# Kernel optimization log

Hardware: AMD Instinct MI355X
Metric: run time of the kernel (lower is better)

## Reference

```python
import jax, jax.numpy as jnp
import numpy as np

EPS = 1e-6

def rmsnorm(x, w):
    # x * rsqrt(mean(x^2, -1) + eps) * w
    ms = jnp.mean(jnp.square(x), axis=-1, keepdims=True)
    return w * (x * jax.lax.rsqrt(ms + EPS))

def setup_inputs() -> dict:
    key = jax.random.key(0)
    ks = jax.random.split(key, 10)
    B, L, T, D, R = 4, 8, 2048, 1024, 64
    h_base = jax.random.normal(ks[0], (B, T, D), dtype=jnp.float32)
    prev_states = jax.random.normal(ks[1], (B, L, T, D), dtype=jnp.float32)
    query = jax.random.normal(ks[2], (D,), dtype=jnp.float32) * 0.02
    gate = jnp.float32(0.5)
    score_w = jnp.ones((D,), dtype=jnp.float32)
    out_w = jnp.ones((D,), dtype=jnp.float32)
    qnorm_w = jnp.ones((D,), dtype=jnp.float32)
    # low-rank query projections (nn.Linear weight layout: [out, in])
    Wd = jax.random.normal(ks[3], (R, D), dtype=jnp.float32) * 0.02
    Wu = jax.random.normal(ks[4], (D, R), dtype=jnp.float32) * 0.02
    # token gate projection
    tg_w = jax.random.normal(ks[5], (1, D), dtype=jnp.float32) * 0.02
    tg_b = jnp.zeros((1,), dtype=jnp.float32)
    return {"h_base": h_base, "prev_states": prev_states, "query": query,
            "gate": gate, "score_w": score_w, "out_w": out_w,
            "qnorm_w": qnorm_w, "Wd": Wd, "Wu": Wu, "tg_w": tg_w, "tg_b": tg_b}

def reference(h_base, prev_states, query, gate, score_w, out_w, qnorm_w, Wd, Wu, tg_w, tg_b):
    sources = prev_states                              # [B,L,T,D]
    normed = rmsnorm(sources, score_w)                 # [B,L,T,D]
    # low-rank input-dependent query: q = query + up(down(qnorm(h)))
    qh = rmsnorm(h_base, qnorm_w)                      # [B,T,D]
    q = query + jnp.einsum('btr,dr->btd', jnp.einsum('btd,rd->btr', qh, Wd), Wu)
    scores = jnp.einsum('btd,bltd->blt', q, normed)    # [B,L,T]
    alpha = jax.nn.softmax(scores, axis=1)             # softmax over depth L
    delta = jnp.einsum('blt,bltd->btd', alpha, sources)
    delta = rmsnorm(delta, out_w)                      # [B,T,D]
    g = gate * jax.nn.sigmoid(h_base @ tg_w.T + tg_b)  # [B,T,1]
    out = h_base + g * delta
    return out, alpha
```

## Files before the change

kernel.cpp:

```cpp
#include <hip/hip_runtime.h>
#include <hip/hip_bf16.h>

#define D_DIM 1024
#define L_DIM 8
#define T_DIM 2048
#define B_DIM 4
#define TOKS  (B_DIM * T_DIM)
#define OUT_ELEMS ((size_t)TOKS * D_DIM)
#define EPSF 1e-6f

typedef __attribute__((ext_vector_type(8)))  short short8_t;
typedef __attribute__((ext_vector_type(16))) float f32x16_t;
typedef __attribute__((ext_vector_type(4)))  float f32x4_t;

__device__ __forceinline__ float dot4v(const f32x4_t& a, const f32x4_t& b) {
    return a.x * b.x + a.y * b.y + a.z * b.z + a.w * b.w;
}

__device__ __forceinline__ unsigned short f2bf(float f) {
    union { __hip_bfloat16 h; unsigned short u; } x;
    x.h = __float2bfloat16(f);
    return x.u;
}

__device__ __forceinline__ float bf2f(unsigned short u) {
    union { unsigned int i; float f; } x;
    x.i = ((unsigned int)u) << 16;
    return x.f;
}

__global__ __launch_bounds__(256) void k_prep(const float* __restrict__ Wd,
                                              const float* __restrict__ qnw,
                                              const float* __restrict__ Wu,
                                              unsigned short* __restrict__ Wdq,
                                              unsigned short* __restrict__ Wubf) {
    int i = (blockIdx.x * 256 + threadIdx.x) * 4;
    float4 wd = *(const float4*)(Wd + i);
    float4 nv = *(const float4*)(qnw + (i & (D_DIM - 1)));
    short4 o1 = make_short4((short)f2bf(wd.x * nv.x), (short)f2bf(wd.y * nv.y),
                            (short)f2bf(wd.z * nv.z), (short)f2bf(wd.w * nv.w));
    *(short4*)(Wdq + i) = o1;
    float4 wu = *(const float4*)(Wu + i);
    short4 o2 = make_short4((short)f2bf(wu.x), (short)f2bf(wu.y),
                            (short)f2bf(wu.z), (short)f2bf(wu.w));
    *(short4*)(Wubf + i) = o2;
}

#define QT_STRIDE 1048
__global__ __launch_bounds__(512) void k_q(const float* __restrict__ h,
                                           const unsigned short* __restrict__ Wdq,
                                           const unsigned short* __restrict__ Wubf,
                                           const float* __restrict__ query,
                                           const float* __restrict__ score_w,
                                           unsigned short* __restrict__ qs) {
    __shared__ __align__(16) char smem[70784];
    float (*c_red)[2][16][64] = (float (*)[2][16][64])smem;
    float (*ssq_red)[32]      = (float (*)[32])(smem + 65536);
    float* scale_sh           = (float*)(smem + 66560);
    unsigned short* r_sw      = (unsigned short*)(smem + 66688);
    unsigned short* qt        = (unsigned short*)smem;

    int tid  = threadIdx.x;
    int w    = tid >> 6;
    int lane = tid & 63;
    int t0   = blockIdx.x * 32;

    f32x16_t acc0, acc1;
#pragma unroll
    for (int r = 0; r < 16; ++r) { acc0[r] = 0.f; acc1[r] = 0.f; }

    int arow = lane & 31;
    int koff = w * 128 + (lane >> 5) * 8;
    const float* hrow = h + (size_t)(t0 + arow) * D_DIM + koff;
    const unsigned short* b0 = Wdq + (size_t)arow * D_DIM + koff;
    const unsigned short* b1 = Wdq + (size_t)(32 + arow) * D_DIM + koff;

    float ssq = 0.f;
#pragma unroll
    for (int s = 0; s < 8; ++s) {
        f32x4_t ha = *(const f32x4_t*)(hrow + s * 16);
        f32x4_t hb = *(const f32x4_t*)(hrow + s * 16 + 4);
        ssq += dot4v(ha, ha) + dot4v(hb, hb);
        short8_t af;
        af[0] = (short)f2bf(ha.x); af[1] = (short)f2bf(ha.y);
        af[2] = (short)f2bf(ha.z); af[3] = (short)f2bf(ha.w);
        af[4] = (short)f2bf(hb.x); af[5] = (short)f2bf(hb.y);
        af[6] = (short)f2bf(hb.z); af[7] = (short)f2bf(hb.w);
        short8_t bf0 = *(const short8_t*)(b0 + s * 16);
        short8_t bf1 = *(const short8_t*)(b1 + s * 16);
        acc0 = __builtin_amdgcn_mfma_f32_32x32x16_bf16(af, bf0, acc0, 0, 0, 0);
        acc1 = __builtin_amdgcn_mfma_f32_32x32x16_bf16(af, bf1, acc1, 0, 0, 0);
    }

    ssq += __shfl_xor(ssq, 32, 64);
    if (lane < 32) ssq_red[w][lane] = ssq;
#pragma unroll
    for (int r = 0; r < 16; ++r) {
        c_red[w][0][r][lane] = acc0[r];
        c_red[w][1][r][lane] = acc1[r];
    }
    __syncthreads();

    if (tid < 32) {
        float s8 = 0.f;
#pragma unroll
        for (int u = 0; u < 8; ++u) s8 += ssq_red[u][tid];
        scale_sh[tid] = rsqrtf(s8 * (1.f / D_DIM) + EPSF);
    }
    __syncthreads();

    for (int idx = tid; idx < 2048; idx += 512) {
        int nj = idx >> 10, rem = idx & 1023, reg = rem >> 6, ln = rem & 63;
        float v = 0.f;
#pragma unroll
        for (int u = 0; u < 8; ++u) v += c_red[u][nj][reg][ln];
        int tk = (reg & 3) + 8 * (reg >> 2) + 4 * (ln >> 5);
        int j  = nj * 32 + (ln & 31);
        v *= scale_sh[tk];
        int byte = (tk * 128 + j * 2) ^ ((tk & 7) << 4);
        r_sw[byte >> 1] = f2bf(v);
    }
    __syncthreads();

    short8_t afr[4];
#pragma unroll
    for (int s = 0; s < 4; ++s) {
        int tk = lane & 31;
        int k  = s * 16 + (lane >> 5) * 8;
        int byte = (tk * 128 + k * 2) ^ ((tk & 7) << 4);
        afr[s] = *(const short8_t*)(&r_sw[byte >> 1]);
    }
    __syncthreads();

#pragma unroll
    for (int i = 0; i < 4; ++i) {
        int n0 = (w * 4 + i) * 32;
        int d  = n0 + (lane & 31);
        f32x16_t c;
#pragma unroll
        for (int r = 0; r < 16; ++r) c[r] = 0.f;
        const unsigned short* bbp = Wubf + (size_t)d * 64 + (lane >> 5) * 8;
#pragma unroll
        for (int s = 0; s < 4; ++s) {
            short8_t bf = *(const short8_t*)(bbp + s * 16);
            c = __builtin_amdgcn_mfma_f32_32x32x16_bf16(afr[s], bf, c, 0, 0, 0);
        }
        float qd  = query[d];
        float swd = score_w[d];
#pragma unroll
        for (int r = 0; r < 16; ++r) {
            int tk = (r & 3) + 8 * (r >> 2) + 4 * (lane >> 5);
            unsigned int v = f2bf((qd + c[r]) * swd);
            unsigned int pv = (unsigned int)__shfl_xor((int)v, 1, 64);
            if ((lane & 1) == 0) {
                unsigned int word = (v & 0xffffu) | (pv << 16);
                *(unsigned int*)&qt[tk * QT_STRIDE + d] = word;
            }
        }
    }
    __syncthreads();

#pragma unroll
    for (int j = 0; j < 8; ++j) {
        int row   = tid >> 4;
        int chunk = (tid & 15) + j * 16;
        short8_t v = *(const short8_t*)&qt[row * QT_STRIDE + chunk * 8];
        *(short8_t*)(qs + (size_t)(t0 + row) * D_DIM + chunk * 8) = v;
    }
}

__global__ __launch_bounds__(256) void k_main(const float* __restrict__ h,
                                              const float* __restrict__ prev,
                                              const unsigned short* __restrict__ qs,
                                              const float* __restrict__ out_w,
                                              const float* __restrict__ tg_w,
                                              const float* __restrict__ gate,
                                              const float* __restrict__ tg_b,
                                              float* __restrict__ out,
                                              float* __restrict__ alpha_out) {
    int lane = threadIdx.x & 63;
    int tok  = (blockIdx.x << 2) + (threadIdx.x >> 6);
    int b    = tok >> 11;
    int t    = tok & (T_DIM - 1);

    const float* pb = prev + ((size_t)(b * L_DIM) * T_DIM + t) * D_DIM + lane * 4;
    f32x4_t p[L_DIM][4];
#pragma unroll
    for (int l = 0; l < L_DIM; ++l)
#pragma unroll
        for (int c = 0; c < 4; ++c)
            p[l][c] = __builtin_nontemporal_load(
                (const f32x4_t*)(pb + (size_t)l * T_DIM * D_DIM + c * 256));

    const float* hb = h + (size_t)tok * D_DIM + lane * 4;
    f32x4_t h4[4], qv[4];
#pragma unroll
    for (int c = 0; c < 4; ++c) h4[c] = *(const f32x4_t*)(hb + c * 256);
#pragma unroll
    for (int c = 0; c < 4; ++c) {
        short4 qr = *(const short4*)(qs + (size_t)tok * D_DIM + c * 256 + lane * 4);
        qv[c].x = bf2f((unsigned short)qr.x);
        qv[c].y = bf2f((unsigned short)qr.y);
        qv[c].z = bf2f((unsigned short)qr.z);
        qv[c].w = bf2f((unsigned short)qr.w);
    }

    float tgp = 0.f;
#pragma unroll
    for (int c = 0; c < 4; ++c) {
        f32x4_t tw = *(const f32x4_t*)(tg_w + c * 256 + lane * 4);
        tgp += dot4v(h4[c], tw);
    }

    float ss[L_DIM], dt[L_DIM];
#pragma unroll
    for (int l = 0; l < L_DIM; ++l) {
        float s = 0.f, d = 0.f;
#pragma unroll
        for (int c = 0; c < 4; ++c) {
            s += dot4v(p[l][c], p[l][c]);
            d += dot4v(p[l][c], qv[c]);
        }
        ss[l] = s; dt[l] = d;
    }

#pragma unroll
    for (int off = 32; off; off >>= 1) {
#pragma unroll
        for (int l = 0; l < L_DIM; ++l) {
            ss[l] += __shfl_xor(ss[l], off, 64);
            dt[l] += __shfl_xor(dt[l], off, 64);
        }
        tgp += __shfl_xor(tgp, off, 64);
    }

    float al[L_DIM], mx = -1e30f;
#pragma unroll
    for (int l = 0; l < L_DIM; ++l) {
        al[l] = dt[l] * rsqrtf(ss[l] * (1.f / D_DIM) + EPSF);
        mx = fmaxf(mx, al[l]);
    }
    float asum = 0.f;
#pragma unroll
    for (int l = 0; l < L_DIM; ++l) { al[l] = __expf(al[l] - mx); asum += al[l]; }
    float inv = 1.f / asum;
#pragma unroll
    for (int l = 0; l < L_DIM; ++l) al[l] *= inv;

    float g = gate[0] / (1.f + __expf(-(tgp + tg_b[0])));

    f32x4_t dl[4];
#pragma unroll
    for (int c = 0; c < 4; ++c) { dl[c].x = 0.f; dl[c].y = 0.f; dl[c].z = 0.f; dl[c].w = 0.f; }
#pragma unroll
    for (int l = 0; l < L_DIM; ++l)
#pragma unroll
        for (int c = 0; c < 4; ++c) {
            dl[c].x += al[l] * p[l][c].x;
            dl[c].y += al[l] * p[l][c].y;
            dl[c].z += al[l] * p[l][c].z;
            dl[c].w += al[l] * p[l][c].w;
        }

    float dss = 0.f;
#pragma unroll
    for (int c = 0; c < 4; ++c) dss += dot4v(dl[c], dl[c]);
#pragma unroll
    for (int off = 32; off; off >>= 1) dss += __shfl_xor(dss, off, 64);
    float dscale = rsqrtf(dss * (1.f / D_DIM) + EPSF);

    float* ob = out + (size_t)tok * D_DIM + lane * 4;
#pragma unroll
    for (int c = 0; c < 4; ++c) {
        f32x4_t ow = *(const f32x4_t*)(out_w + c * 256 + lane * 4);
        f32x4_t o;
        o.x = h4[c].x + g * dl[c].x * dscale * ow.x;
        o.y = h4[c].y + g * dl[c].y * dscale * ow.y;
        o.z = h4[c].z + g * dl[c].z * dscale * ow.z;
        o.w = h4[c].w + g * dl[c].w * dscale * ow.w;
        __builtin_nontemporal_store(o, (f32x4_t*)(ob + c * 256));
    }

    if (lane < L_DIM)
        alpha_out[(size_t)b * (L_DIM * T_DIM) + (size_t)lane * T_DIM + t] = al[lane];
}

extern "C" void kernel_launch(void* const* d_in, const int* in_sizes, int n_in,
                              void* d_out, int out_size, void* d_ws, size_t ws_size,
                              hipStream_t stream) {
    (void)in_sizes; (void)n_in; (void)out_size; (void)ws_size;
    const float* h       = (const float*)d_in[0];
    const float* prev    = (const float*)d_in[1];
    const float* query   = (const float*)d_in[2];
    const float* gate    = (const float*)d_in[3];
    const float* score_w = (const float*)d_in[4];
    const float* out_w   = (const float*)d_in[5];
    const float* qnw     = (const float*)d_in[6];
    const float* Wd      = (const float*)d_in[7];
    const float* Wu      = (const float*)d_in[8];
    const float* tg_w    = (const float*)d_in[9];
    const float* tg_b    = (const float*)d_in[10];

    float* out   = (float*)d_out;
    float* alpha = out + OUT_ELEMS;

    unsigned short* qsbuf = (unsigned short*)d_ws;
    unsigned short* Wdq   = qsbuf + OUT_ELEMS;
    unsigned short* Wubf  = Wdq + (size_t)64 * D_DIM;

    k_prep<<<64, 256, 0, stream>>>(Wd, qnw, Wu, Wdq, Wubf);
    k_q<<<TOKS / 32, 512, 0, stream>>>(h, Wdq, Wubf, query, score_w, qsbuf);
    k_main<<<TOKS / 4, 256, 0, stream>>>(h, prev, qsbuf, out_w, tg_w, gate, tg_b, out, alpha);
}
```

Measured before the change: 87.10 us.

## Fuse weight prep, query projection and main depth-attention into one kernel

Merges the three launches into a single kernel. Each 512-thread block computes the low-rank query for 32 tokens into shared memory, then each wave processes 4 of those tokens' depth attention, reading q from LDS instead of a global bf16 buffer. Weight conversion to bf16 (with qnorm scaling) is now done inline per block from fp32 weights, which removes the prep kernel and the q round-trip through global memory. In exchange, every block re-reads and converts Wd/Wu, and occupancy drops: 64KB+ of LDS per block and only 256 blocks, so less latency hiding on the streaming prev_states loads.

After: 84.30 us. 3.2% less time.

```diff
diff --git a/kernel.cpp b/kernel.cpp
--- a/kernel.cpp
+++ b/kernel.cpp
@@ -29,36 +29,26 @@
     return x.f;
 }
 
-__global__ __launch_bounds__(256) void k_prep(const float* __restrict__ Wd,
-                                              const float* __restrict__ qnw,
-                                              const float* __restrict__ Wu,
-                                              unsigned short* __restrict__ Wdq,
-                                              unsigned short* __restrict__ Wubf) {
-    int i = (blockIdx.x * 256 + threadIdx.x) * 4;
-    float4 wd = *(const float4*)(Wd + i);
-    float4 nv = *(const float4*)(qnw + (i & (D_DIM - 1)));
-    short4 o1 = make_short4((short)f2bf(wd.x * nv.x), (short)f2bf(wd.y * nv.y),
-                            (short)f2bf(wd.z * nv.z), (short)f2bf(wd.w * nv.w));
-    *(short4*)(Wdq + i) = o1;
-    float4 wu = *(const float4*)(Wu + i);
-    short4 o2 = make_short4((short)f2bf(wu.x), (short)f2bf(wu.y),
-                            (short)f2bf(wu.z), (short)f2bf(wu.w));
-    *(short4*)(Wubf + i) = o2;
-}
-
-#define QT_STRIDE 1048
-__global__ __launch_bounds__(512) void k_q(const float* __restrict__ h,
-                                           const unsigned short* __restrict__ Wdq,
-                                           const unsigned short* __restrict__ Wubf,
-                                           const float* __restrict__ query,
-                                           const float* __restrict__ score_w,
-                                           unsigned short* __restrict__ qs) {
-    __shared__ __align__(16) char smem[70784];
+__global__ __launch_bounds__(512) void k_all(const float* __restrict__ h,
+                                             const float* __restrict__ prev,
+                                             const float* __restrict__ query,
+                                             const float* __restrict__ score_w,
+                                             const float* __restrict__ out_w,
+                                             const float* __restrict__ tg_w,
+                                             const float* __restrict__ gate,
+                                             const float* __restrict__ tg_b,
+                                             const float* __restrict__ qnw,
+                                             const float* __restrict__ Wd,
+                                             const float* __restrict__ Wu,
+                                             float* __restrict__ out,
+                                             float* __restrict__ alpha_out) {
+    __shared__ __align__(16) char smem[65536];
     float (*c_red)[2][16][64] = (float (*)[2][16][64])smem;
-    float (*ssq_red)[32]      = (float (*)[32])(smem + 65536);
-    float* scale_sh           = (float*)(smem + 66560);
-    unsigned short* r_sw      = (unsigned short*)(smem + 66688);
-    unsigned short* qt        = (unsigned short*)smem;
+    unsigned short* qt = (unsigned short*)smem;
+
+    __shared__ float ssq_red[8][32];
+    __shared__ float scale_sh[32];
+    __shared__ unsigned short r_sw[2048];
 
     int tid  = threadIdx.x;
     int w    = tid >> 6;
@@ -72,8 +62,9 @@
     int arow = lane & 31;
     int koff = w * 128 + (lane >> 5) * 8;
     const float* hrow = h + (size_t)(t0 + arow) * D_DIM + koff;
-    const unsigned short* b0 = Wdq + (size_t)arow * D_DIM + koff;
-    const unsigned short* b1 = Wdq + (size_t)(32 + arow) * D_DIM + koff;
+    const float* w0r  = Wd + (size_t)arow * D_DIM + koff;
+    const float* w1r  = Wd + (size_t)(32 + arow) * D_DIM + koff;
+    const float* nr   = qnw + koff;
 
     float ssq = 0.f;
 #pragma unroll
@@ -86,8 +77,22 @@
         af[2] = (short)f2bf(ha.z); af[3] = (short)f2bf(ha.w);
         af[4] = (short)f2bf(hb.x); af[5] = (short)f2bf(hb.y);
         af[6] = (short)f2bf(hb.z); af[7] = (short)f2bf(hb.w);
-        short8_t bf0 = *(const short8_t*)(b0 + s * 16);
-        short8_t bf1 = *(const short8_t*)(b1 + s * 16);
+        f32x4_t na = *(const f32x4_t*)(nr + s * 16);
+        f32x4_t nb = *(const f32x4_t*)(nr + s * 16 + 4);
+        f32x4_t wa = *(const f32x4_t*)(w0r + s * 16);
+        f32x4_t wb = *(const f32x4_t*)(w0r + s * 16 + 4);
+        short8_t bf0;
+        bf0[0] = (short)f2bf(wa.x * na.x); bf0[1] = (short)f2bf(wa.y * na.y);
+        bf0[2] = (short)f2bf(wa.z * na.z); bf0[3] = (short)f2bf(wa.w * na.w);
+        bf0[4] = (short)f2bf(wb.x * nb.x); bf0[5] = (short)f2bf(wb.y * nb.y);
+        bf0[6] = (short)f2bf(wb.z * nb.z); bf0[7] = (short)f2bf(wb.w * nb.w);
+        f32x4_t va = *(const f32x4_t*)(w1r + s * 16);
+        f32x4_t vb = *(const f32x4_t*)(w1r + s * 16 + 4);
+        short8_t bf1;
+        bf1[0] = (short)f2bf(va.x * na.x); bf1[1] = (short)f2bf(va.y * na.y);
+        bf1[2] = (short)f2bf(va.z * na.z); bf1[3] = (short)f2bf(va.w * na.w);
+        bf1[4] = (short)f2bf(vb.x * nb.x); bf1[5] = (short)f2bf(vb.y * nb.y);
+        bf1[6] = (short)f2bf(vb.z * nb.z); bf1[7] = (short)f2bf(vb.w * nb.w);
         acc0 = __builtin_amdgcn_mfma_f32_32x32x16_bf16(af, bf0, acc0, 0, 0, 0);
         acc1 = __builtin_amdgcn_mfma_f32_32x32x16_bf16(af, bf1, acc1, 0, 0, 0);
     }
@@ -139,10 +144,16 @@
         f32x16_t c;
 #pragma unroll
         for (int r = 0; r < 16; ++r) c[r] = 0.f;
-        const unsigned short* bbp = Wubf + (size_t)d * 64 + (lane >> 5) * 8;
+        const float* wup = Wu + (size_t)d * 64 + (lane >> 5) * 8;
 #pragma unroll
         for (int s = 0; s < 4; ++s) {
-            short8_t bf = *(const short8_t*)(bbp + s * 16);
+            f32x4_t ua = *(const f32x4_t*)(wup + s * 16);
+            f32x4_t ub = *(const f32x4_t*)(wup + s * 16 + 4);
+            short8_t bf;
+            bf[0] = (short)f2bf(ua.x); bf[1] = (short)f2bf(ua.y);
+            bf[2] = (short)f2bf(ua.z); bf[3] = (short)f2bf(ua.w);
+            bf[4] = (short)f2bf(ub.x); bf[5] = (short)f2bf(ub.y);
+            bf[6] = (short)f2bf(ub.z); bf[7] = (short)f2bf(ub.w);
             c = __builtin_amdgcn_mfma_f32_32x32x16_bf16(afr[s], bf, c, 0, 0, 0);
         }
         float qd  = query[d];
@@ -154,141 +165,128 @@
             unsigned int pv = (unsigned int)__shfl_xor((int)v, 1, 64);
             if ((lane & 1) == 0) {
                 unsigned int word = (v & 0xffffu) | (pv << 16);
-                *(unsigned int*)&qt[tk * QT_STRIDE + d] = word;
+                *(unsigned int*)&qt[tk * 1024 + d] = word;
             }
         }
     }
     __syncthreads();
 
-#pragma unroll
-    for (int j = 0; j < 8; ++j) {
-        int row   = tid >> 4;
-        int chunk = (tid & 15) + j * 16;
-        short8_t v = *(const short8_t*)&qt[row * QT_STRIDE + chunk * 8];
-        *(short8_t*)(qs + (size_t)(t0 + row) * D_DIM + chunk * 8) = v;
-    }
-}
-
-__global__ __launch_bounds__(256) void k_main(const float* __restrict__ h,
-                                              const float* __restrict__ prev,
-                                              const unsigned short* __restrict__ qs,
-                                              const float* __restrict__ out_w,
-                                              const float* __restrict__ tg_w,
-                                              const float* __restrict__ gate,
-                                              const float* __restrict__ tg_b,
-                                              float* __restrict__ out,
-                                              float* __restrict__ alpha_out) {
-    int lane = threadIdx.x & 63;
-    int tok  = (blockIdx.x << 2) + (threadIdx.x >> 6);
-    int b    = tok >> 11;
-    int t    = tok & (T_DIM - 1);
-
-    const float* pb = prev + ((size_t)(b * L_DIM) * T_DIM + t) * D_DIM + lane * 4;
-    f32x4_t p[L_DIM][4];
-#pragma unroll
-    for (int l = 0; l < L_DIM; ++l)
-#pragma unroll
-        for (int c = 0; c < 4; ++c)
-            p[l][c] = __builtin_nontemporal_load(
-                (const f32x4_t*)(pb + (size_t)l * T_DIM * D_DIM + c * 256));
-
-    const float* hb = h + (size_t)tok * D_DIM + lane * 4;
-    f32x4_t h4[4], qv[4];
-#pragma unroll
-    for (int c = 0; c < 4; ++c) h4[c] = *(const f32x4_t*)(hb + c * 256);
-#pragma unroll
-    for (int c = 0; c < 4; ++c) {
-        short4 qr = *(const short4*)(qs + (size_t)tok * D_DIM + c * 256 + lane * 4);
-        qv[c].x = bf2f((unsigned short)qr.x);
-        qv[c].y = bf2f((unsigned short)qr.y);
-        qv[c].z = bf2f((unsigned short)qr.z);
-        qv[c].w = bf2f((unsigned short)qr.w);
-    }
-
-    float tgp = 0.f;
-#pragma unroll
-    for (int c = 0; c < 4; ++c) {
-        f32x4_t tw = *(const f32x4_t*)(tg_w + c * 256 + lane * 4);
-        tgp += dot4v(h4[c], tw);
-    }
-
-    float ss[L_DIM], dt[L_DIM];
-#pragma unroll
-    for (int l = 0; l < L_DIM; ++l) {
-        float s = 0.f, d = 0.f;
+    int bb    = t0 >> 11;
+    int tloc0 = t0 & (T_DIM - 1);
+
+#pragma unroll 1
+    for (int i = 0; i < 4; ++i) {
+        int tt  = w * 4 + i;
+        int tok = t0 + tt;
+        int t   = tloc0 + tt;
+
+        const float* pb = prev + ((size_t)(bb * L_DIM) * T_DIM + t) * D_DIM + lane * 4;
+        f32x4_t p[L_DIM][4];
+#pragma unroll
+        for (int l = 0; l < L_DIM; ++l)
+#pragma unroll
+            for (int c = 0; c < 4; ++c)
+                p[l][c] = __builtin_nontemporal_load(
+                    (const f32x4_t*)(pb + (size_t)l * T_DIM * D_DIM + c * 256));
+
+        const float* hb = h + (size_t)tok * D_DIM + lane * 4;
+        f32x4_t h4[4], qv[4];
+#pragma unroll
+        for (int c = 0; c < 4; ++c) h4[c] = *(const f32x4_t*)(hb + c * 256);
 #pragma unroll
         for (int c = 0; c < 4; ++c) {
-            s += dot4v(p[l][c], p[l][c]);
-            d += dot4v(p[l][c], qv[c]);
-        }
-        ss[l] = s; dt[l] = d;
-    }
-
-#pragma unroll
-    for (int off = 32; off; off >>= 1) {
+            short4 qr = *(const short4*)&qt[tt * 1024 + c * 256 + lane * 4];
+            qv[c].x = bf2f((unsigned short)qr.x);
+            qv[c].y = bf2f((unsigned short)qr.y);
+            qv[c].z = bf2f((unsigned short)qr.z);
+            qv[c].w = bf2f((unsigned short)qr.w);
+        }
+
+        float tgp = 0.f;
+#pragma unroll
+        for (int c = 0; c < 4; ++c) {
+            f32x4_t tw = *(const f32x4_t*)(tg_w + c * 256 + lane * 4);
+            tgp += dot4v(h4[c], tw);
+        }
+
+        float ss[L_DIM], dt[L_DIM];
 #pragma unroll
         for (int l = 0; l < L_DIM; ++l) {
-            ss[l] += __shfl_xor(ss[l], off, 64);
-            dt[l] += __shfl_xor(dt[l], off, 64);
-        }
-        tgp += __shfl_xor(tgp, off, 64);
-    }
-
-    float al[L_DIM], mx = -1e30f;
-#pragma unroll
-    for (int l = 0; l < L_DIM; ++l) {
-        al[l] = dt[l] * rsqrtf(ss[l] * (1.f / D_DIM) + EPSF);
-        mx = fmaxf(mx, al[l]);
-    }
-    float asum = 0.f;
-#pragma unroll
-    for (int l = 0; l < L_DIM; ++l) { al[l] = __expf(al[l] - mx); asum += al[l]; }
-    float inv = 1.f / asum;
-#pragma unroll
-    for (int l = 0; l < L_DIM; ++l) al[l] *= inv;
-
-    float g = gate[0] / (1.f + __expf(-(tgp + tg_b[0])));
-
-    f32x4_t dl[4];
-#pragma unroll
-    for (int c = 0; c < 4; ++c) { dl[c].x = 0.f; dl[c].y = 0.f; dl[c].z = 0.f; dl[c].w = 0.f; }
-#pragma unroll
-    for (int l = 0; l < L_DIM; ++l)
+            float s = 0.f, d = 0.f;
+#pragma unroll
+            for (int c = 0; c < 4; ++c) {
+                s += dot4v(p[l][c], p[l][c]);
+                d += dot4v(p[l][c], qv[c]);
+            }
+            ss[l] = s; dt[l] = d;
+        }
+
+#pragma unroll
+        for (int off = 32; off; off >>= 1) {
+#pragma unroll
+            for (int l = 0; l < L_DIM; ++l) {
+                ss[l] += __shfl_xor(ss[l], off, 64);
+                dt[l] += __shfl_xor(dt[l], off, 64);
+            }
+            tgp += __shfl_xor(tgp, off, 64);
+        }
+
+        float al[L_DIM], mx = -1e30f;
+#pragma unroll
+        for (int l = 0; l < L_DIM; ++l) {
+            al[l] = dt[l] * rsqrtf(ss[l] * (1.f / D_DIM) + EPSF);
+            mx = fmaxf(mx, al[l]);
+        }
+        float asum = 0.f;
+#pragma unroll
+        for (int l = 0; l < L_DIM; ++l) { al[l] = __expf(al[l] - mx); asum += al[l]; }
+        float inv = 1.f / asum;
+#pragma unroll
+        for (int l = 0; l < L_DIM; ++l) al[l] *= inv;
+
+        float g = gate[0] / (1.f + __expf(-(tgp + tg_b[0])));
+
+        f32x4_t dl[4];
+#pragma unroll
+        for (int c = 0; c < 4; ++c) { dl[c].x = 0.f; dl[c].y = 0.f; dl[c].z = 0.f; dl[c].w = 0.f; }
+#pragma unroll
+        for (int l = 0; l < L_DIM; ++l)
+#pragma unroll
+            for (int c = 0; c < 4; ++c) {
+                dl[c].x += al[l] * p[l][c].x;
+                dl[c].y += al[l] * p[l][c].y;
+                dl[c].z += al[l] * p[l][c].z;
+                dl[c].w += al[l] * p[l][c].w;
+            }
+
+        float dss = 0.f;
+#pragma unroll
+        for (int c = 0; c < 4; ++c) dss += dot4v(dl[c], dl[c]);
+#pragma unroll
+        for (int off = 32; off; off >>= 1) dss += __shfl_xor(dss, off, 64);
+        float dscale = rsqrtf(dss * (1.f / D_DIM) + EPSF);
+
+        float* ob = out + (size_t)tok * D_DIM + lane * 4;
 #pragma unroll
         for (int c = 0; c < 4; ++c) {
-            dl[c].x += al[l] * p[l][c].x;
-            dl[c].y += al[l] * p[l][c].y;
-            dl[c].z += al[l] * p[l][c].z;
-            dl[c].w += al[l] * p[l][c].w;
-        }
-
-    float dss = 0.f;
-#pragma unroll
-    for (int c = 0; c < 4; ++c) dss += dot4v(dl[c], dl[c]);
-#pragma unroll
-    for (int off = 32; off; off >>= 1) dss += __shfl_xor(dss, off, 64);
-    float dscale = rsqrtf(dss * (1.f / D_DIM) + EPSF);
-
-    float* ob = out + (size_t)tok * D_DIM + lane * 4;
-#pragma unroll
-    for (int c = 0; c < 4; ++c) {
-        f32x4_t ow = *(const f32x4_t*)(out_w + c * 256 + lane * 4);
-        f32x4_t o;
-        o.x = h4[c].x + g * dl[c].x * dscale * ow.x;
-        o.y = h4[c].y + g * dl[c].y * dscale * ow.y;
-        o.z = h4[c].z + g * dl[c].z * dscale * ow.z;
-        o.w = h4[c].w + g * dl[c].w * dscale * ow.w;
-        __builtin_nontemporal_store(o, (f32x4_t*)(ob + c * 256));
-    }
-
-    if (lane < L_DIM)
-        alpha_out[(size_t)b * (L_DIM * T_DIM) + (size_t)lane * T_DIM + t] = al[lane];
+            f32x4_t ow = *(const f32x4_t*)(out_w + c * 256 + lane * 4);
+            f32x4_t o;
+            o.x = h4[c].x + g * dl[c].x * dscale * ow.x;
+            o.y = h4[c].y + g * dl[c].y * dscale * ow.y;
+            o.z = h4[c].z + g * dl[c].z * dscale * ow.z;
+            o.w = h4[c].w + g * dl[c].w * dscale * ow.w;
+            __builtin_nontemporal_store(o, (f32x4_t*)(ob + c * 256));
+        }
+
+        if (lane < L_DIM)
+            alpha_out[(size_t)bb * (L_DIM * T_DIM) + (size_t)lane * T_DIM + t] = al[lane];
+    }
 }
 
 extern "C" void kernel_launch(void* const* d_in, const int* in_sizes, int n_in,
                               void* d_out, int out_size, void* d_ws, size_t ws_size,
                               hipStream_t stream) {
-    (void)in_sizes; (void)n_in; (void)out_size; (void)ws_size;
+    (void)in_sizes; (void)n_in; (void)out_size; (void)d_ws; (void)ws_size;
     const float* h       = (const float*)d_in[0];
     const float* prev    = (const float*)d_in[1];
     const float* query   = (const float*)d_in[2];
@@ -304,11 +302,6 @@
     float* out   = (float*)d_out;
     float* alpha = out + OUT_ELEMS;
 
-    unsigned short* qsbuf = (unsigned short*)d_ws;
-    unsigned short* Wdq   = qsbuf + OUT_ELEMS;
-    unsigned short* Wubf  = Wdq + (size_t)64 * D_DIM;
-
-    k_prep<<<64, 256, 0, stream>>>(Wd, qnw, Wu, Wdq, Wubf);
-    k_q<<<TOKS / 32, 512, 0, stream>>>(h, Wdq, Wubf, query, score_w, qsbuf);
-    k_main<<<TOKS / 4, 256, 0, stream>>>(h, prev, qsbuf, out_w, tg_w, gate, tg_b, out, alpha);
-}
+    k_all<<<TOKS / 32, 512, 0, stream>>>(h, prev, query, score_w, out_w, tg_w,
+                                         gate, tg_b, qnw, Wd, Wu, out, alpha);
+}
```
